# Optimization experiments

Measured on AMD Instinct MI355X. Metric: run time of the kernel, lower is better.

The kernel has to match this reference:

```python
import jax, jax.numpy as jnp
import numpy as np

B, N, D, H = 4, 2048, 512, 8
DH = D // H
EPS = 1e-6


def setup_inputs() -> dict:
    key = jax.random.key(0)
    ks = jax.random.split(key, 12)
    s = 1.0 / np.sqrt(D)
    return {
        "x": jax.random.normal(ks[0], (B, N, D), jnp.float32),
        "attn_bias": jax.random.normal(ks[1], (B, 1, N, N), jnp.float32),
        "Wq": jax.random.normal(ks[2], (D, D), jnp.float32) * s,
        "bq": jnp.zeros((D,), jnp.float32),
        "Wk": jax.random.normal(ks[3], (D, D), jnp.float32) * s,
        "bk": jnp.zeros((D,), jnp.float32),
        "Wv": jax.random.normal(ks[4], (D, D), jnp.float32) * s,
        "bv": jnp.zeros((D,), jnp.float32),
        "Wo": jax.random.normal(ks[5], (D, D), jnp.float32) * s,
        "bo": jnp.zeros((D,), jnp.float32),
        "q_gamma": jnp.ones((DH,), jnp.float32),
        "q_beta": jnp.zeros((DH,), jnp.float32),
        "k_gamma": jnp.ones((DH,), jnp.float32),
        "k_beta": jnp.zeros((DH,), jnp.float32),
    }


def _layernorm(x, gamma, beta):
    mu = jnp.mean(x, axis=-1, keepdims=True)
    var = jnp.var(x, axis=-1, keepdims=True)
    return (x - mu) * jax.lax.rsqrt(var + EPS) * gamma + beta


def reference(x, attn_bias, Wq, bq, Wk, bk, Wv, bv, Wo, bo,
              q_gamma, q_beta, k_gamma, k_beta):
    b, n, d = x.shape
    # project and split heads: (B, H, N, DH)
    def heads(W, bias):
        return (x @ W.T + bias).reshape(b, n, H, DH).transpose(0, 2, 1, 3)
    q = heads(Wq, bq)
    k = heads(Wk, bk)
    v = heads(Wv, bv)
    q = _layernorm(q, q_gamma, q_beta)
    k = _layernorm(k, k_gamma, k_beta)
    scores = jnp.einsum('bhqd,bhkd->bhqk', q, k) / np.sqrt(DH)
    scores = scores + attn_bias  # (B,1,N,N) broadcasts over heads
    attn = jax.nn.softmax(scores, axis=-1)
    out = jnp.einsum('bhqk,bhkd->bhqd', attn, v)
    out = out.transpose(0, 2, 1, 3).reshape(b, n, d)
    return out @ Wo.T + bo
```

## Files before the change

### kernel.cpp

```cpp
#include <hip/hip_runtime.h>

typedef __attribute__((ext_vector_type(8))) short short8;
typedef __attribute__((ext_vector_type(4))) float f32x4;
typedef __attribute__((ext_vector_type(4))) int i32x4;
typedef __attribute__((ext_vector_type(4))) unsigned short u16x4;
typedef __attribute__((ext_vector_type(8))) unsigned short u16x8;
typedef __attribute__((ext_vector_type(2))) unsigned int u32x2;

#define B_  4
#define N_  2048
#define D_  512
#define H_  8
#define DH_ 64
#define M_  (B_ * N_)

__device__ __forceinline__ unsigned short f2bf(float f) {
    union { float f; unsigned u; } un; un.f = f;
    unsigned r = un.u + 0x7FFFu + ((un.u >> 16) & 1u);
    return (unsigned short)(r >> 16);
}
__device__ __forceinline__ float exp2fast(float x) {
#if __has_builtin(__builtin_amdgcn_exp2f)
    return __builtin_amdgcn_exp2f(x);
#else
    float r; asm("v_exp_f32 %0, %1" : "=v"(r) : "v"(x)); return r;
#endif
}
__device__ __forceinline__ unsigned cvtpk_bf16(float lo, float hi) {
    unsigned r;
    asm("v_cvt_pk_bf16_f32 %0, %1, %2" : "=v"(r) : "v"(lo), "v"(hi));
    return r;
}
__device__ __forceinline__ float max3f(float a, float b, float c) {
    return fmaxf(fmaxf(a, b), c);
}

typedef __attribute__((address_space(1))) const void gvoid;
typedef __attribute__((address_space(3))) void svoid;
__device__ __forceinline__ void load16_lds(const void* g, void* s) {
    __builtin_amdgcn_global_load_lds((gvoid*)g, (svoid*)s, 16, 0, 0);
}

__global__ __launch_bounds__(256) void cvt_all(
    const float* __restrict__ x,
    const float* __restrict__ W0, const float* __restrict__ W1,
    const float* __restrict__ W2, const float* __restrict__ W3,
    unsigned short* __restrict__ xb, unsigned short* __restrict__ Wb) {
    const int bx = blockIdx.x;
    const float* src;
    unsigned short* dst;
    int i;
    if (bx < 4096) {
        src = x; dst = xb;
        i = (bx * 256 + (int)threadIdx.x) * 4;
    } else {
        const int r = bx - 4096;
        const int sel = r >> 8;
        src = (sel == 0) ? W0 : (sel == 1) ? W1 : (sel == 2) ? W2 : W3;
        dst = Wb + (size_t)sel * D_ * D_;
        i = ((r & 255) * 256 + (int)threadIdx.x) * 4;
    }
    f32x4 v = *(const f32x4*)(src + i);
    u16x4 o;
    o[0] = f2bf(v[0]); o[1] = f2bf(v[1]); o[2] = f2bf(v[2]); o[3] = f2bf(v[3]);
    *(u16x4*)(dst + i) = o;
}

template <bool F32OUT, bool LNF>
__global__ __launch_bounds__(256, 2) void gemm_nt(
    const unsigned short* __restrict__ A,
    const unsigned short* __restrict__ W,
    const float* __restrict__ Bv0,
    const float* __restrict__ Bv1,
    const float* __restrict__ Bv2,
    const float* __restrict__ g0, const float* __restrict__ be0,
    const float* __restrict__ g1, const float* __restrict__ be1,
    unsigned short* __restrict__ outb,
    float* __restrict__ outf)
{
    const int mt = blockIdx.x;
    const int nt = blockIdx.y;
    const int sel = nt >> 2;
    const unsigned short* Wp = W + (size_t)sel * D_ * D_;
    const float* Bv = (sel == 0) ? Bv0 : (sel == 1) ? Bv1 : Bv2;
    const int n0 = (nt & 3) * 128;

    __shared__ __align__(16) unsigned short As[128 * 32];
    __shared__ __align__(16) unsigned short Bs[128 * 32];

    const int tid = threadIdx.x;
    const int w   = tid >> 6;
    const int l   = tid & 63;
    const int l15 = l & 15;
    const int qd  = l >> 4;
    const int wr  = w >> 1;
    const int wc  = w & 1;

    int srow[2], scol[2];
#pragma unroll
    for (int c = 0; c < 2; ++c) {
        const int g   = (w * 2 + c) * 64 + l;
        const int row = g >> 2;
        srow[c] = row;
        scol[c] = ((g & 3) ^ (row & 3)) * 8;
    }

    f32x4 acc[4][4];
#pragma unroll
    for (int i = 0; i < 4; ++i)
#pragma unroll
        for (int j = 0; j < 4; ++j)
            acc[i][j] = (f32x4){0.f, 0.f, 0.f, 0.f};

    const int swz = qd ^ (l15 & 3);

    for (int k0 = 0; k0 < D_; k0 += 32) {
        __syncthreads();
#pragma unroll
        for (int c = 0; c < 2; ++c) {
            load16_lds(A  + (size_t)(mt * 128 + srow[c]) * D_ + k0 + scol[c],
                       As + (w * 2 + c) * 512);
            load16_lds(Wp + (size_t)(n0 + srow[c]) * D_ + k0 + scol[c],
                       Bs + (w * 2 + c) * 512);
        }
        __syncthreads();

        short8 af[4], bfr[4];
#pragma unroll
        for (int rt = 0; rt < 4; ++rt)
            af[rt] = *(const short8*)&As[(wr * 64 + rt * 16 + l15) * 32 + swz * 8];
#pragma unroll
        for (int ct = 0; ct < 4; ++ct)
            bfr[ct] = *(const short8*)&Bs[(wc * 64 + ct * 16 + l15) * 32 + swz * 8];
#pragma unroll
        for (int rt = 0; rt < 4; ++rt)
#pragma unroll
            for (int ct = 0; ct < 4; ++ct)
                acc[rt][ct] = __builtin_amdgcn_mfma_f32_16x16x32_bf16(
                    af[rt], bfr[ct], acc[rt][ct], 0, 0, 0);
    }

    const float* gam = (sel == 0) ? g0 : g1;
    const float* bet = (sel == 0) ? be0 : be1;
    float gv[4], bv2[4];
    if (LNF) {
#pragma unroll
        for (int ct = 0; ct < 4; ++ct) { gv[ct] = gam[ct * 16 + l15]; bv2[ct] = bet[ct * 16 + l15]; }
    }

#pragma unroll
    for (int rt = 0; rt < 4; ++rt) {
        float v[4][4];
#pragma unroll
        for (int ct = 0; ct < 4; ++ct) {
            const float bias = Bv[n0 + wc * 64 + ct * 16 + l15];
#pragma unroll
            for (int r = 0; r < 4; ++r) v[ct][r] = acc[rt][ct][r] + bias;
        }
        if (LNF && sel < 2) {
#pragma unroll
            for (int r = 0; r < 4; ++r) {
                float s  = v[0][r] + v[1][r] + v[2][r] + v[3][r];
                float s2 = v[0][r]*v[0][r] + v[1][r]*v[1][r] + v[2][r]*v[2][r] + v[3][r]*v[3][r];
#pragma unroll
                for (int o = 1; o <= 8; o <<= 1) {
                    s  += __shfl_xor(s, o);
                    s2 += __shfl_xor(s2, o);
                }
                const float mu  = s * 0.015625f;
                const float var = s2 * 0.015625f - mu * mu;
                const float rs  = rsqrtf(var + 1e-6f);
#pragma unroll
                for (int ct = 0; ct < 4; ++ct)
                    v[ct][r] = (v[ct][r] - mu) * rs * gv[ct] + bv2[ct];
            }
        }
#pragma unroll
        for (int ct = 0; ct < 4; ++ct) {
            const int col  = n0 + wc * 64 + ct * 16 + l15;
            const int row0 = mt * 128 + wr * 64 + rt * 16 + qd * 4;
#pragma unroll
            for (int r = 0; r < 4; ++r) {
                const size_t oidx = (size_t)(row0 + r) * D_ + col;
                if (F32OUT) outf[oidx] = v[ct][r];
                else        outb[(size_t)sel * M_ * D_ + oidx] = f2bf(v[ct][r]);
            }
        }
    }
}

__global__ __launch_bounds__(256) void pack_kv(
    const unsigned short* __restrict__ K, const unsigned short* __restrict__ V,
    unsigned short* __restrict__ Kt, unsigned short* __restrict__ Vt2)
{
    const int nt = blockIdx.x, b = blockIdx.y;
    const int tid = threadIdx.x;
    __shared__ __align__(16) unsigned short Vl[64][520];

#pragma unroll
    for (int i = 0; i < 16; ++i) {
        const int c = i * 256 + tid;
        const int row = c >> 6, ch = c & 63;
        const size_t srow = ((size_t)(b * N_ + nt * 64 + row)) * D_ + ch * 8;
        i32x4 kd = *(const i32x4*)(K + srow);
        const int h = ch >> 3, dc = ch & 7;
        *(i32x4*)(Kt + ((((size_t)(b * 8 + h) * 32 + nt) * 64 + row) * 64) + dc * 8) = kd;
        i32x4 vd = *(const i32x4*)(V + srow);
        *(i32x4*)&Vl[row][ch * 8] = vd;
    }
    __syncthreads();
#pragma unroll
    for (int i = 0; i < 16; ++i) {
        const int c = i * 256 + tid;
        const int h = c >> 9, r = c & 511;
        const int dh = r >> 3, kc = r & 7;
        u16x8 o;
#pragma unroll
        for (int j = 0; j < 8; ++j) o[j] = Vl[kc * 8 + j][h * 64 + dh];
        *(u16x8*)(Vt2 + ((((size_t)(b * 8 + h) * 32 + nt) * 64 + dh) * 64) + kc * 8) = o;
    }
}

__global__ __launch_bounds__(512, 4) void attn11(
    const unsigned short* __restrict__ Qm,
    const unsigned short* __restrict__ Kt,
    const unsigned short* __restrict__ Vt2,
    const float* __restrict__ Bias,
    unsigned short* __restrict__ AO)
{
    const int qt = blockIdx.x;
    const int h  = blockIdx.y;
    const int b  = blockIdx.z;
    const int w  = threadIdx.x >> 6;
    const int l  = threadIdx.x & 63;
    const int l15 = l & 15;
    const int qd  = l >> 4;
    const int q0 = qt * 128 + w * 16;
    const float L2E = 1.4426950408889634f;

    __shared__ __align__(16) unsigned char smem[51200];
    unsigned short* PwB = (unsigned short*)(smem + 32768) + w * 16 * 72;

    const int c    = w * 64 + l;
    const int srow = c >> 3;
    const int sg   = (c & 7) ^ (srow & 7);
    const int soff = srow * 64 + sg * 8;
    const int sc16 = c * 16;

    short8 qf[2];
#pragma unroll
    for (int hf = 0; hf < 2; ++hf)
        qf[hf] = *(const short8*)(Qm +
            (size_t)(b * N_ + q0 + l15) * D_ + h * DH_ + hf * 32 + qd * 8);

    f32x4 Ot[4];
#pragma unroll
    for (int rt = 0; rt < 4; ++rt) Ot[rt] = (f32x4){0.f, 0.f, 0.f, 0.f};
    float m_i = -3.0e38f;
    f32x4 li4 = (f32x4){0.f, 0.f, 0.f, 0.f};

    const unsigned short* Ktile0 = Kt  + (((size_t)(b * 8 + h) * 32) * 64) * 64;
    const unsigned short* Vtile0 = Vt2 + (((size_t)(b * 8 + h) * 32) * 64) * 64;
    const float* biasQ = Bias + ((size_t)b * N_ + q0 + l15) * N_;

    load16_lds(Ktile0 + soff, smem + sc16);
    load16_lds(Vtile0 + soff, smem + 8192 + sc16);
    f32x4 brA[4], brB[4];
#pragma unroll
    for (int rt = 0; rt < 4; ++rt)
        brA[rt] = *(const f32x4*)(biasQ + rt * 16 + qd * 4);
    asm volatile("s_waitcnt vmcnt(0)" ::: "memory");

#define ATTN_ITER(KT, CUR, BRC, BRN) do {                                      \
    unsigned char* Kbc = smem + (CUR) * 16384;                                 \
    unsigned char* Vbc = Kbc + 8192;                                           \
    asm volatile("s_waitcnt vmcnt(4)" ::: "memory");                           \
    __builtin_amdgcn_s_barrier();                                              \
    __builtin_amdgcn_sched_barrier(0);                                         \
    if ((KT) < 31) {                                                           \
        const unsigned short* Kn = Ktile0 + (size_t)((KT) + 1) * 4096;         \
        const unsigned short* Vn = Vtile0 + (size_t)((KT) + 1) * 4096;         \
        unsigned char* KbN = smem + (((CUR) ^ 1)) * 16384;                     \
        load16_lds(Kn + soff, KbN + sc16);                                     \
        load16_lds(Vn + soff, KbN + 8192 + sc16);                              \
    }                                                                          \
    asm volatile("" ::: "memory");       \
    {                                                                          \
        const float* Bn = biasQ + (size_t)(((KT) < 31) ? (KT) + 1 : 31) * 64;  \
        _Pragma("unroll")                                                      \
        for (int rt = 0; rt < 4; ++rt)                                         \
            BRN[rt] = *(const f32x4*)(Bn + rt * 16 + qd * 4);                  \
    }                                                                          \
    short8 kf[4][2];                                                           \
    _Pragma("unroll")                                                          \
    for (int rt = 0; rt < 4; ++rt) {                                           \
        const int kv = rt * 16 + l15;                                          \
        _Pragma("unroll")                                                      \
        for (int hf = 0; hf < 2; ++hf) {                                       \
            const int cidx = (hf * 4 + qd) ^ (kv & 7);                         \
            kf[rt][hf] = *(const short8*)(Kbc + kv * 128 + cidx * 16);         \
        }                                                                      \
    }                                                                          \
    f32x4 St[4];                                                               \
    __builtin_amdgcn_s_setprio(1);                                             \
    _Pragma("unroll")                                                          \
    for (int rt = 0; rt < 4; ++rt) {                                           \
        f32x4 v = (f32x4){0.f, 0.f, 0.f, 0.f};                                 \
        v = __builtin_amdgcn_mfma_f32_16x16x32_bf16(kf[rt][0], qf[0], v, 0, 0, 0); \
        v = __builtin_amdgcn_mfma_f32_16x16x32_bf16(kf[rt][1], qf[1], v, 0, 0, 0); \
        St[rt] = v;                                                            \
    }                                                                          \
    __builtin_amdgcn_s_setprio(0);                                             \
    short8 vf[4][2];                                                           \
    _Pragma("unroll")                                                          \
    for (int rt = 0; rt < 4; ++rt) {                                           \
        const int dh = rt * 16 + l15;                                          \
        _Pragma("unroll")                                                      \
        for (int hf = 0; hf < 2; ++hf) {                                       \
            const int cidx = (hf * 4 + qd) ^ (dh & 7);                         \
            vf[rt][hf] = *(const short8*)(Vbc + dh * 128 + cidx * 16);         \
        }                                                                      \
    }                                                                          \
    {                                                                          \
                      \
        f32x4 sv[4];                                                           \
        _Pragma("unroll")                                                      \
        for (int rt = 0; rt < 4; ++rt)                                         \
            sv[rt] = St[rt] * 0.125f + BRC[rt];                                \
                                                  \
        float mx0 = max3f(sv[0][0], sv[0][1], sv[0][2]);                       \
        float mx1 = max3f(sv[0][3], sv[1][0], sv[1][1]);                       \
        float mx2 = max3f(sv[1][2], sv[1][3], sv[2][0]);                       \
        float mx3 = max3f(sv[2][1], sv[2][2], sv[2][3]);                       \
        mx0 = max3f(mx0, sv[3][0], sv[3][1]);                                  \
        mx1 = max3f(mx1, sv[3][2], sv[3][3]);                                  \
        float mx = fmaxf(max3f(mx0, mx1, mx2), mx3);                           \
        mx = fmaxf(mx, __shfl_xor(mx, 16));                                    \
        mx = fmaxf(mx, __shfl_xor(mx, 32));                                    \
                \
        if (__any(mx > m_i + 8.0f)) {                                          \
            const float mnew  = fmaxf(m_i, mx);                                \
            const float alpha = exp2fast((m_i - mnew) * L2E);                  \
            m_i = mnew;                                                        \
            li4 *= alpha;                                                      \
            _Pragma("unroll")                                                  \
            for (int rt = 0; rt < 4; ++rt) Ot[rt] *= alpha;                    \
        }                                                                      \
        const float mL = m_i * L2E;                                            \
        f32x4 p[4];                                                            \
        _Pragma("unroll")                                                      \
        for (int rt = 0; rt < 4; ++rt) {                                       \
            f32x4 e = sv[rt] * L2E - mL;                           \
            p[rt][0] = exp2fast(e[0]); p[rt][1] = exp2fast(e[1]);              \
            p[rt][2] = exp2fast(e[2]); p[rt][3] = exp2fast(e[3]);              \
        }                                                                      \
        li4 += (p[0] + p[1]) + (p[2] + p[3]);                                  \
        _Pragma("unroll")                                                      \
        for (int rt = 0; rt < 4; ++rt) {                                       \
            u32x2 pw;                                                          \
            pw[0] = cvtpk_bf16(p[rt][0], p[rt][1]);                            \
            pw[1] = cvtpk_bf16(p[rt][2], p[rt][3]);                            \
            *(u32x2*)&PwB[l15 * 72 + rt * 16 + qd * 4] = pw;                   \
        }                                                                      \
    }                                                                          \
    short8 pf[2];                                                              \
    _Pragma("unroll")                                                          \
    for (int hf = 0; hf < 2; ++hf)                                             \
        pf[hf] = *(const short8*)&PwB[l15 * 72 + hf * 32 + qd * 8];            \
    __builtin_amdgcn_s_setprio(1);                                             \
    _Pragma("unroll")                                                          \
    for (int rt = 0; rt < 4; ++rt) {                                           \
        Ot[rt] = __builtin_amdgcn_mfma_f32_16x16x32_bf16(vf[rt][0], pf[0], Ot[rt], 0, 0, 0); \
        Ot[rt] = __builtin_amdgcn_mfma_f32_16x16x32_bf16(vf[rt][1], pf[1], Ot[rt], 0, 0, 0); \
    }                                                                          \
    __builtin_amdgcn_s_setprio(0);                                             \
} while (0)

    for (int kt2 = 0; kt2 < 16; ++kt2) {
        ATTN_ITER(kt2 * 2,     0, brA, brB);
        ATTN_ITER(kt2 * 2 + 1, 1, brB, brA);
    }
#undef ATTN_ITER

    float l_i = (li4[0] + li4[1]) + (li4[2] + li4[3]);
    l_i += __shfl_xor(l_i, 16);
    l_i += __shfl_xor(l_i, 32);
    const float inv = 1.f / l_i;
    const int q = q0 + l15;
#pragma unroll
    for (int rt = 0; rt < 4; ++rt) {
        u16x4 ob;
#pragma unroll
        for (int r = 0; r < 4; ++r) ob[r] = f2bf(Ot[rt][r] * inv);
        *(u16x4*)(AO + (size_t)(b * N_ + q) * D_ + h * DH_ + rt * 16 + qd * 4) = ob;
    }
}

extern "C" void kernel_launch(void* const* d_in, const int* in_sizes, int n_in,
                              void* d_out, int out_size, void* d_ws, size_t ws_size,
                              hipStream_t stream) {
    const float* x  = (const float*)d_in[0];
    const float* ab = (const float*)d_in[1];
    const float* Wq = (const float*)d_in[2];
    const float* bq = (const float*)d_in[3];
    const float* Wk = (const float*)d_in[4];
    const float* bk = (const float*)d_in[5];
    const float* Wv = (const float*)d_in[6];
    const float* bv = (const float*)d_in[7];
    const float* Wo = (const float*)d_in[8];
    const float* bo = (const float*)d_in[9];
    const float* qg = (const float*)d_in[10];
    const float* qb = (const float*)d_in[11];
    const float* kg = (const float*)d_in[12];
    const float* kb = (const float*)d_in[13];

    unsigned short* xb  = (unsigned short*)d_ws;
    unsigned short* Wb  = xb  + (size_t)M_ * D_;
    unsigned short* Y   = Wb  + (size_t)4 * D_ * D_;
    unsigned short* Kt  = Y   + (size_t)3 * M_ * D_;
    unsigned short* Vt2 = Kt  + (size_t)M_ * D_;
    unsigned short* AO  = Vt2 + (size_t)M_ * D_;
    float* out = (float*)d_out;

    cvt_all<<<dim3(5120), dim3(256), 0, stream>>>(x, Wq, Wk, Wv, Wo, xb, Wb);

    gemm_nt<false, true><<<dim3(64, 12), dim3(256), 0, stream>>>(
        xb, Wb, bq, bk, bv, qg, qb, kg, kb, Y, nullptr);

    pack_kv<<<dim3(32, 4), dim3(256), 0, stream>>>(
        Y + (size_t)M_ * D_, Y + (size_t)2 * M_ * D_, Kt, Vt2);

    attn11<<<dim3(16, 8, 4), dim3(512), 0, stream>>>(
        Y, Kt, Vt2, ab, AO);

    gemm_nt<true, false><<<dim3(64, 4), dim3(256), 0, stream>>>(
        AO, Wb + (size_t)3 * D_ * D_, bo, bo, bo,
        nullptr, nullptr, nullptr, nullptr, nullptr, out);
}
```

Baseline: 257.1 us.

## Keep softmax probabilities in registers by permuting V layout to match MFMA

The P tile is no longer written to shared memory and read back in the B-operand layout. The packed bf16 probabilities from the score MFMA output are fed directly to the PV MFMA. To keep this correct, pack_kv now stores V with a permuted key-column order so the reduction index matches the register order of P. This removes LDS writes and reads per iteration and shrinks shared memory from 51200 to 32768 bytes, which may allow higher occupancy.

Measured after the change: 257.1 us. No clear change (+0.0%).

```diff
diff --git a/kernel.cpp b/kernel.cpp
--- a/kernel.cpp
+++ b/kernel.cpp
@@ -214,14 +214,20 @@
         const int c = i * 256 + tid;
         const int h = c >> 9, r = c & 511;
         const int dh = r >> 3, kc = r & 7;
-        u16x8 o;
-#pragma unroll
-        for (int j = 0; j < 8; ++j) o[j] = Vl[kc * 8 + j][h * 64 + dh];
-        *(u16x8*)(Vt2 + ((((size_t)(b * 8 + h) * 32 + nt) * 64 + dh) * 64) + kc * 8) = o;
-    }
-}
-
-__global__ __launch_bounds__(512, 4) void attn11(
+        u16x4 o0, o1;
+#pragma unroll
+        for (int j = 0; j < 4; ++j) o0[j] = Vl[kc * 8 + j][h * 64 + dh];
+#pragma unroll
+        for (int j = 0; j < 4; ++j) o1[j] = Vl[kc * 8 + 4 + j][h * 64 + dh];
+        const int t = kc >> 1;
+        const int col0 = (t & 2) * 16 + (kc & 1) * 16 + (t & 1) * 4;
+        const size_t rowbase = ((((size_t)(b * 8 + h) * 32 + nt) * 64 + dh) * 64);
+        *(u16x4*)(Vt2 + rowbase + col0)     = o0;
+        *(u16x4*)(Vt2 + rowbase + col0 + 8) = o1;
+    }
+}
+
+__global__ __launch_bounds__(512, 4) void attn12(
     const unsigned short* __restrict__ Qm,
     const unsigned short* __restrict__ Kt,
     const unsigned short* __restrict__ Vt2,
@@ -238,8 +244,7 @@
     const int q0 = qt * 128 + w * 16;
     const float L2E = 1.4426950408889634f;
 
-    __shared__ __align__(16) unsigned char smem[51200];
-    unsigned short* PwB = (unsigned short*)(smem + 32768) + w * 16 * 72;
+    __shared__ __align__(16) unsigned char smem[32768];
 
     const int c    = w * 64 + l;
     const int srow = c >> 3;
@@ -321,13 +326,12 @@
             vf[rt][hf] = *(const short8*)(Vbc + dh * 128 + cidx * 16);         \
         }                                                                      \
     }                                                                          \
+    unsigned wq[4][2];                                                         \
     {                                                                          \
-                      \
         f32x4 sv[4];                                                           \
         _Pragma("unroll")                                                      \
         for (int rt = 0; rt < 4; ++rt)                                         \
             sv[rt] = St[rt] * 0.125f + BRC[rt];                                \
-                                                  \
         float mx0 = max3f(sv[0][0], sv[0][1], sv[0][2]);                       \
         float mx1 = max3f(sv[0][3], sv[1][0], sv[1][1]);                       \
         float mx2 = max3f(sv[1][2], sv[1][3], sv[2][0]);                       \
@@ -337,7 +341,6 @@
         float mx = fmaxf(max3f(mx0, mx1, mx2), mx3);                           \
         mx = fmaxf(mx, __shfl_xor(mx, 16));                                    \
         mx = fmaxf(mx, __shfl_xor(mx, 32));                                    \
-                \
         if (__any(mx > m_i + 8.0f)) {                                          \
             const float mnew  = fmaxf(m_i, mx);                                \
             const float alpha = exp2fast((m_i - mnew) * L2E);                  \
@@ -350,28 +353,28 @@
         f32x4 p[4];                                                            \
         _Pragma("unroll")                                                      \
         for (int rt = 0; rt < 4; ++rt) {                                       \
-            f32x4 e = sv[rt] * L2E - mL;                           \
+            f32x4 e = sv[rt] * L2E - mL;                                       \
             p[rt][0] = exp2fast(e[0]); p[rt][1] = exp2fast(e[1]);              \
             p[rt][2] = exp2fast(e[2]); p[rt][3] = exp2fast(e[3]);              \
         }                                                                      \
         li4 += (p[0] + p[1]) + (p[2] + p[3]);                                  \
         _Pragma("unroll")                                                      \
         for (int rt = 0; rt < 4; ++rt) {                                       \
-            u32x2 pw;                                                          \
-            pw[0] = cvtpk_bf16(p[rt][0], p[rt][1]);                            \
-            pw[1] = cvtpk_bf16(p[rt][2], p[rt][3]);                            \
-            *(u32x2*)&PwB[l15 * 72 + rt * 16 + qd * 4] = pw;                   \
+            wq[rt][0] = cvtpk_bf16(p[rt][0], p[rt][1]);                        \
+            wq[rt][1] = cvtpk_bf16(p[rt][2], p[rt][3]);                        \
         }                                                                      \
     }                                                                          \
-    short8 pf[2];                                                              \
-    _Pragma("unroll")                                                          \
-    for (int hf = 0; hf < 2; ++hf)                                             \
-        pf[hf] = *(const short8*)&PwB[l15 * 72 + hf * 32 + qd * 8];            \
+                           \
+    union { unsigned u[4]; short8 s; } pk0, pk1;                               \
+    pk0.u[0] = wq[0][0]; pk0.u[1] = wq[0][1];                                  \
+    pk0.u[2] = wq[1][0]; pk0.u[3] = wq[1][1];                                  \
+    pk1.u[0] = wq[2][0]; pk1.u[1] = wq[2][1];                                  \
+    pk1.u[2] = wq[3][0]; pk1.u[3] = wq[3][1];                                  \
     __builtin_amdgcn_s_setprio(1);                                             \
     _Pragma("unroll")                                                          \
     for (int rt = 0; rt < 4; ++rt) {                                           \
-        Ot[rt] = __builtin_amdgcn_mfma_f32_16x16x32_bf16(vf[rt][0], pf[0], Ot[rt], 0, 0, 0); \
-        Ot[rt] = __builtin_amdgcn_mfma_f32_16x16x32_bf16(vf[rt][1], pf[1], Ot[rt], 0, 0, 0); \
+        Ot[rt] = __builtin_amdgcn_mfma_f32_16x16x32_bf16(vf[rt][0], pk0.s, Ot[rt], 0, 0, 0); \
+        Ot[rt] = __builtin_amdgcn_mfma_f32_16x16x32_bf16(vf[rt][1], pk1.s, Ot[rt], 0, 0, 0); \
     }                                                                          \
     __builtin_amdgcn_s_setprio(0);                                             \
 } while (0)
@@ -430,7 +433,7 @@
     pack_kv<<<dim3(32, 4), dim3(256), 0, stream>>>(
         Y + (size_t)M_ * D_, Y + (size_t)2 * M_ * D_, Kt, Vt2);
 
-    attn11<<<dim3(16, 8, 4), dim3(512), 0, stream>>>(
+    attn12<<<dim3(16, 8, 4), dim3(512), 0, stream>>>(
         Y, Kt, Vt2, ab, AO);
 
     gemm_nt<true, false><<<dim3(64, 4), dim3(256), 0, stream>>>(
```
